# Optimization experiments

Hardware: AMD Instinct MI355X
Metric: run time of the kernel (lower is better)

The kernel has to match this reference:

```python
import jax, jax.numpy as jnp
import numpy as np

NUM_GROUPS, GROUP_SIZE, D_MODEL = 8, 4096, 1024
NUM_EXPERTS = 64
EXPERT_CAPACITY = 1024  # capacity_factor 2: 2 * total_tokens / num_experts


def setup_inputs() -> dict:
    key = jax.random.key(0)
    k1, k2, k3 = jax.random.split(key, 3)
    x = jax.random.normal(k1, (NUM_GROUPS, GROUP_SIZE, D_MODEL), dtype=jnp.float32)
    gate_kernel = jax.random.normal(k2, (D_MODEL, NUM_EXPERTS), dtype=jnp.float32) * 0.1
    gate_bias = jax.random.normal(k3, (NUM_EXPERTS,), dtype=jnp.float32) * 0.01
    temperature = jnp.ones((1,), dtype=jnp.float32)
    return {
        "x": x,
        "gate_kernel": gate_kernel,
        "gate_bias": gate_bias,
        "temperature": temperature,
        "expert_capacity": EXPERT_CAPACITY,
    }


def reference(x, gate_kernel, gate_bias, temperature, expert_capacity):
    # x: [G, S, D]; gate_kernel: [D, E]
    G, S, _ = x.shape
    E = gate_kernel.shape[1]

    router_logits = jnp.einsum("gsd,de->gse", x, gate_kernel) + gate_bias  # [G, S, E]
    safe_temp = jnp.maximum(temperature, 0.1)  # [1]
    router_probs = jax.nn.softmax(router_logits / safe_temp, axis=-1)  # [G, S, E]

    # Per-expert top-k over all flattened tokens.
    flat_probs = router_probs.transpose(2, 0, 1).reshape(E, G * S)  # [E, G*S]
    scores, token_indices = jax.lax.top_k(flat_probs, k=expert_capacity)  # [E, C]

    group_indices = token_indices // S  # [E, C]
    pos_indices = token_indices % S  # [E, C]
    expert_ids = jnp.broadcast_to(jnp.arange(E)[:, None], scores.shape)  # [E, C]

    # use_mask_routing=True path: scatter into capacity-limited dense masks.
    expert_masks = jnp.zeros((E, G, S), dtype=jnp.bool_).at[
        expert_ids, group_indices, pos_indices].set(True)
    weight_masks = jnp.zeros((E, G, S), dtype=x.dtype).at[
        expert_ids, group_indices, pos_indices].set(scores)

    loss = jnp.asarray(0.0, dtype=x.dtype)  # training=False
    return expert_masks, weight_masks, loss
```

## Files before the change

### kernel.cpp

```cpp
#include <hip/hip_runtime.h>
#include <math.h>

#define NG 8
#define SEQ 4096
#define DM 1024
#define NE 64
#define GS (NG * SEQ)
#define KSEL 1024
#define MASK_ELEMS (NE * GS)
#define SEG 16
#define SEGLEN (GS / SEG)
#define CAP 2048
#define CAP2 16384

typedef __attribute__((ext_vector_type(8))) short short8;
typedef __attribute__((ext_vector_type(4))) float f32x4;

__device__ __forceinline__ unsigned short f2bf(float v) {
  unsigned u = __float_as_uint(v);
  return (unsigned short)((u + 0x7FFFu + ((u >> 16) & 1u)) >> 16);
}
__device__ __forceinline__ float bf2f(unsigned short h) {
  return __uint_as_float(((unsigned)h) << 16);
}

__global__ __launch_bounds__(256)
void k_split(const float* __restrict__ w, unsigned short* __restrict__ wph,
             unsigned short* __restrict__ wpm, unsigned* __restrict__ zbase) {
  const int t = blockIdx.x * 256 + threadIdx.x;
  if (t < NE * 256 + NE) zbase[t] = 0u;
  const int k = t >> 6, e = t & 63;
  float v = w[t];
  unsigned short h = f2bf(v); float r = v - bf2f(h);
  const int tile = k >> 5, g = (k >> 3) & 3, j = k & 7;
  const int cb = e >> 4, lrow = e & 15;
  const size_t o = (size_t)(tile * 4 + cb) * 512 + (g * 16 + lrow) * 8 + j;
  wph[o] = h; wpm[o] = f2bf(r);
}

__global__ __launch_bounds__(256, 2)
void k_gemm_softmax(const float* __restrict__ x,
                    const unsigned short* __restrict__ wph,
                    const unsigned short* __restrict__ wpm,
                    const float* __restrict__ bias, const float* __restrict__ temp,
                    float* __restrict__ probsT) {
  __shared__ float Lt[4][64][68];
  float (*Pt)[68] = (float (*)[68])&Lt[0][0][0];

  const int tid = threadIdx.x;
  const int w = tid >> 6, lane = tid & 63;
  const int lrow = lane & 15, g = lane >> 4;
  const int m0 = blockIdx.x * 64;

  int irow[4], jcol[4];
  {
    union { unsigned short u[8]; short8 v; } ar, on;
#pragma unroll
    for (int j = 0; j < 8; ++j) { ar.u[j] = f2bf((float)lrow); on.u[j] = 0x3F80u; }
    f32x4 z = {0.f, 0.f, 0.f, 0.f};
    f32x4 p1 = __builtin_amdgcn_mfma_f32_16x16x32_bf16(ar.v, on.v, z, 0, 0, 0);
    f32x4 p2 = __builtin_amdgcn_mfma_f32_16x16x32_bf16(on.v, ar.v, z, 0, 0, 0);
#pragma unroll
    for (int b = 0; b < 4; ++b) {
      irow[b] = ((int)p1[b]) >> 5;
      jcol[b] = ((int)p2[b]) >> 5;
    }
  }

  f32x4 acc[4][4];
#pragma unroll
  for (int rf = 0; rf < 4; ++rf)
#pragma unroll
    for (int cb = 0; cb < 4; ++cb) acc[rf][cb] = (f32x4){0.f, 0.f, 0.f, 0.f};

  const int boff = lane * 8;
  const int T0 = w * 8;

  f32x4 aP[4][2], aQ[4][2];
  short8 bhP[4], bmP[4], bhQ[4], bmQ[4];

#define LOADA_(T, ar)                                                                \
  {                                                                                  \
    _Pragma("unroll")                                                                \
    for (int rf = 0; rf < 4; ++rf) {                                                 \
      const f32x4* ap = (const f32x4*)(x + (size_t)(m0 + rf * 16 + lrow) * DM +      \
                                       (T) * 32 + g * 8);                            \
      ar[rf][0] = ap[0]; ar[rf][1] = ap[1];                                          \
    }                                                                                \
  }

#define LOADB_(T, bh, bm)                                                            \
  {                                                                                  \
    _Pragma("unroll")                                                                \
    for (int cb = 0; cb < 4; ++cb) {                                                 \
      const size_t bo = (size_t)((T) * 4 + cb) * 512 + boff;                         \
      bh[cb] = *(const short8*)(wph + bo);                                           \
      bm[cb] = *(const short8*)(wpm + bo);                                           \
    }                                                                                \
  }

#define SPLIT_MFMA(ar, bh, bm)                                                       \
  {                                                                                  \
    _Pragma("unroll")                                                                \
    for (int rf = 0; rf < 4; ++rf) {                                                 \
      union { unsigned short u[8]; short8 v; } ah, am;                               \
      _Pragma("unroll")                                                              \
      for (int j = 0; j < 8; ++j) {                                                  \
        float v0 = (j < 4) ? ar[rf][0][j] : ar[rf][1][j - 4];                        \
        unsigned short h_ = f2bf(v0);                                                \
        ah.u[j] = h_; am.u[j] = f2bf(v0 - bf2f(h_));                                 \
      }                                                                              \
      _Pragma("unroll")                                                              \
      for (int cb = 0; cb < 4; ++cb) {                                               \
        acc[rf][cb] = __builtin_amdgcn_mfma_f32_16x16x32_bf16(ah.v, bh[cb],          \
                                                              acc[rf][cb], 0, 0, 0); \
        acc[rf][cb] = __builtin_amdgcn_mfma_f32_16x16x32_bf16(am.v, bh[cb],          \
                                                              acc[rf][cb], 0, 0, 0); \
        acc[rf][cb] = __builtin_amdgcn_mfma_f32_16x16x32_bf16(ah.v, bm[cb],          \
                                                              acc[rf][cb], 0, 0, 0); \
      }                                                                              \
    }                                                                                \
  }

  LOADA_(T0, aP);
  LOADB_(T0, bhP, bmP);
#pragma unroll
  for (int t = 0; t < 8; t += 2) {
    LOADA_(T0 + t + 1, aQ);
    LOADB_(T0 + t + 1, bhQ, bmQ);
    SPLIT_MFMA(aP, bhP, bmP);
    if (t + 2 < 8) {
      LOADA_(T0 + t + 2, aP);
      LOADB_(T0 + t + 2, bhP, bmP);
    }
    SPLIT_MFMA(aQ, bhQ, bmQ);
  }

#undef LOADA_
#undef LOADB_
#undef SPLIT_MFMA

#pragma unroll
  for (int rf = 0; rf < 4; ++rf)
#pragma unroll
    for (int cb = 0; cb < 4; ++cb)
#pragma unroll
      for (int b = 0; b < 4; ++b)
        Lt[w][rf * 16 + irow[b]][cb * 16 + jcol[b]] = acc[rf][cb][b];
  __syncthreads();

  float pr[16];
  const int tk = tid >> 2, q = tid & 3;
  {
    float st = temp[0];
    if (st < 0.1f) st = 0.1f;
    const float inv_t = 1.0f / st;
    float l[16];
    float mx = -1.0e30f;
#pragma unroll
    for (int j = 0; j < 16; ++j) {
      const int e = q * 16 + j;
      l[j] = (Lt[0][tk][e] + Lt[1][tk][e] + Lt[2][tk][e] + Lt[3][tk][e] + bias[e]) *
             inv_t;
      mx = fmaxf(mx, l[j]);
    }
    mx = fmaxf(mx, __shfl_xor(mx, 1));
    mx = fmaxf(mx, __shfl_xor(mx, 2));
    float p[16], s = 0.0f;
#pragma unroll
    for (int j = 0; j < 16; ++j) { p[j] = __expf(l[j] - mx); s += p[j]; }
    s += __shfl_xor(s, 1);
    s += __shfl_xor(s, 2);
    const float invs = 1.0f / s;
#pragma unroll
    for (int j = 0; j < 16; ++j) pr[j] = p[j] * invs;
  }
  __syncthreads();
#pragma unroll
  for (int j = 0; j < 16; ++j) Pt[q * 16 + j][tk] = pr[j];
  __syncthreads();

  {
    const int e = tid >> 2, qq = tid & 3;
    float* dst = probsT + (size_t)e * GS + m0 + qq * 16;
#pragma unroll
    for (int c2 = 0; c2 < 4; ++c2)
      *(float4*)(dst + c2 * 4) = *(const float4*)(&Pt[e][qq * 16 + c2 * 4]);
  }
}

__device__ __forceinline__ void pick_scan(const unsigned* __restrict__ bins,
                                          unsigned r_in, unsigned& bucket,
                                          unsigned& r_out, unsigned* res) {
  __syncthreads();
  const int tid = threadIdx.x;
  if (tid < 64) {
    uint4 b = ((const uint4*)bins)[tid];
    unsigned s3 = b.w, s2 = b.z + s3, s1 = b.y + s2, s0 = b.x + s1;
    unsigned suf = s0;
#pragma unroll
    for (int off = 1; off < 64; off <<= 1) {
      unsigned t = __shfl_down(suf, off);
      if (tid + off < 64) suf += t;
    }
    unsigned above = suf - s0;
    unsigned inc0 = above + s0, inc1 = above + s1, inc2 = above + s2, inc3 = above + s3;
    if (inc3 >= r_in && inc3 - b.w < r_in) { res[0] = 4 * tid + 3; res[1] = r_in - (inc3 - b.w); }
    if (inc2 >= r_in && inc2 - b.z < r_in) { res[0] = 4 * tid + 2; res[1] = r_in - (inc2 - b.z); }
    if (inc1 >= r_in && inc1 - b.y < r_in) { res[0] = 4 * tid + 1; res[1] = r_in - (inc1 - b.y); }
    if (inc0 >= r_in && inc0 - b.x < r_in) { res[0] = 4 * tid + 0; res[1] = r_in - (inc0 - b.x); }
  }
  __syncthreads();
  bucket = res[0];
  r_out = res[1];
}

__global__ __launch_bounds__(256)
void k_hist0(const float* __restrict__ probsT, unsigned* __restrict__ ghist0) {
  __shared__ unsigned h[4][256];
  const int tid = threadIdx.x, wv = tid >> 6;
  const int e = blockIdx.x >> 4;
  const int seg = blockIdx.x & (SEG - 1);
  h[0][tid] = 0; h[1][tid] = 0; h[2][tid] = 0; h[3][tid] = 0;
  __syncthreads();
  const float4* col = (const float4*)(probsT + (size_t)e * GS + seg * SEGLEN);
#pragma unroll
  for (int i = 0; i < SEGLEN / 1024; ++i) {
    float4 v = col[i * 256 + tid];
    atomicAdd(&h[wv][__float_as_uint(v.x) >> 24], 1u);
    atomicAdd(&h[wv][__float_as_uint(v.y) >> 24], 1u);
    atomicAdd(&h[wv][__float_as_uint(v.z) >> 24], 1u);
    atomicAdd(&h[wv][__float_as_uint(v.w) >> 24], 1u);
  }
  __syncthreads();
  unsigned c = h[0][tid] + h[1][tid] + h[2][tid] + h[3][tid];
  if (c) atomicAdd(&ghist0[e * 256 + tid], c);
}

__global__ __launch_bounds__(256)
void k_compact(const float* __restrict__ probsT, const unsigned* __restrict__ ghist0,
               unsigned* __restrict__ cCnt, int* __restrict__ cIdx,
               float* __restrict__ cKey) {
  __shared__ unsigned res[2];
  __shared__ unsigned locN, basePos;
  __shared__ int locIdx[2048];
  __shared__ float locKey[2048];
  const int tid = threadIdx.x;
  const int e = blockIdx.x >> 4;
  const int seg = blockIdx.x & (SEG - 1);

  if (tid == 0) locN = 0u;
  unsigned b0, r0;
  pick_scan(ghist0 + e * 256, KSEL, b0, r0, res);
  const unsigned blo = (b0 == 0u) ? 0u : (b0 - 1u);

  const float* col = probsT + (size_t)e * GS + seg * SEGLEN;
  for (int i = 0; i < SEGLEN / 256; ++i) {
    const int t = i * 256 + tid;
    const float p = col[t];
    if ((__float_as_uint(p) >> 24) >= blo) {
      unsigned pos = atomicAdd(&locN, 1u);
      locIdx[pos] = seg * SEGLEN + t;
      locKey[pos] = p;
    }
  }
  __syncthreads();
  if (tid == 0) basePos = locN ? atomicAdd(&cCnt[e], locN) : 0u;
  __syncthreads();
  const unsigned n = locN, bp = basePos;
  for (unsigned i = tid; i < n; i += 256) {
    const unsigned gp = bp + i;
    if (gp < CAP2) {
      cIdx[(size_t)e * CAP2 + gp] = locIdx[i];
      cKey[(size_t)e * CAP2 + gp] = locKey[i];
    }
  }
}

__global__ __launch_bounds__(256)
void k_select2(const unsigned* __restrict__ ghist0, const unsigned* __restrict__ cCnt,
               const int* __restrict__ cIdx, const float* __restrict__ cKey,
               const float* __restrict__ temp, unsigned* __restrict__ defCnt,
               unsigned* __restrict__ candCnt, int* __restrict__ candIdx,
               float* __restrict__ thrHiA) {
  __shared__ unsigned res[2];
  __shared__ unsigned h[4][256];
  __shared__ unsigned hs[256];
  __shared__ unsigned nd, nc;
  const int tid = threadIdx.x, wv = tid >> 6;
  const int e = blockIdx.x;
  const int cnt = (int)min(cCnt[e], (unsigned)CAP2);

  unsigned b0, r;
  pick_scan(ghist0 + e * 256, KSEL, b0, r, res);
  unsigned pfx = b0 << 24;

  for (int pass = 1; pass < 4; ++pass) {
    const int shift = 24 - 8 * pass;
    const unsigned hm = 0xFFFFFFFFu << (shift + 8);
    for (int i = tid; i < 1024; i += 256) ((unsigned*)h)[i] = 0u;
    __syncthreads();
    for (int i = tid; i < cnt; i += 256) {
      unsigned key = __float_as_uint(cKey[(size_t)e * CAP2 + i]);
      if ((key & hm) == (pfx & hm)) atomicAdd(&h[wv][(key >> shift) & 255], 1u);
    }
    __syncthreads();
    hs[tid] = h[0][tid] + h[1][tid] + h[2][tid] + h[3][tid];
    unsigned b, rn;
    pick_scan(hs, r, b, rn, res);
    pfx |= b << shift;
    r = rn;
  }

  const float thrv = __uint_as_float(pfx);
  float st = temp[0];
  if (st < 0.1f) st = 0.1f;
  const float rel = 2.0e-3f / st;
  const float hi = thrv * (1.0f + rel);
  const float lo = thrv * (1.0f - rel);
  if (tid == 0) thrHiA[e] = hi;

  if (tid == 0) { nd = 0u; nc = 0u; }
  __syncthreads();
  for (int i = tid; i < cnt; i += 256) {
    const float p = cKey[(size_t)e * CAP2 + i];
    const int t = cIdx[(size_t)e * CAP2 + i];
    if (p > hi) {
      atomicAdd(&nd, 1u);
    } else if (p >= lo) {
      unsigned pos = atomicAdd(&nc, 1u);
      if (pos < CAP) candIdx[e * CAP + pos] = t;
    }
  }
  __syncthreads();
  if (tid == 0) {
    defCnt[e] = nd;
    candCnt[e] = min(nc, (unsigned)CAP);
  }
}

__global__ __launch_bounds__(256)
void k_repair(const float* __restrict__ x, const float* __restrict__ w,
              const float* __restrict__ bias, const float* __restrict__ temp,
              const unsigned* __restrict__ candCnt, const int* __restrict__ candIdx,
              double* __restrict__ candKey) {
  __shared__ double red[4][64];
  const int e = blockIdx.x >> 4;
  const int chunk = blockIdx.x & 15;
  const int tid = threadIdx.x;
  const int ee = tid & 63, q = tid >> 6;
  const int cnt = (int)min(candCnt[e], (unsigned)CAP);

  double st = (double)temp[0];
  if (st < 0.1) st = 0.1;
  const double inv_t = 1.0 / st;

  for (int i = chunk; i < cnt; i += 16) {
    const int t = candIdx[e * CAP + i];
    const float* xr = x + (size_t)t * DM;
    double s0 = 0.0, s1 = 0.0, s2 = 0.0, s3 = 0.0;
    const int kb = q * 256;
    for (int k = kb; k < kb + 256; k += 4) {
      s0 += (double)xr[k + 0] * (double)w[(size_t)(k + 0) * NE + ee];
      s1 += (double)xr[k + 1] * (double)w[(size_t)(k + 1) * NE + ee];
      s2 += (double)xr[k + 2] * (double)w[(size_t)(k + 2) * NE + ee];
      s3 += (double)xr[k + 3] * (double)w[(size_t)(k + 3) * NE + ee];
    }
    red[q][ee] = (s0 + s1) + (s2 + s3);
    __syncthreads();
    if (tid < 64) {
      double l = (red[0][tid] + red[1][tid] + red[2][tid] + red[3][tid] +
                  (double)bias[tid]) * inv_t;
      double m = l;
#pragma unroll
      for (int off = 1; off < 64; off <<= 1) m = fmax(m, __shfl_xor(m, off));
      double ex = exp(l - m);
      double ss = ex;
#pragma unroll
      for (int off = 1; off < 64; off <<= 1) ss += __shfl_xor(ss, off);
      if (tid == e) candKey[e * CAP + i] = ex / ss;
    }
    __syncthreads();
  }
}

__global__ __launch_bounds__(256)
void k_scatter(const float* __restrict__ probsT, const float* __restrict__ thrHiA,
               float* __restrict__ out) {
  const int gid = blockIdx.x * 256 + threadIdx.x;
  const int base = gid * 4;
  const int e = base >> 15;
  float4 p = *(const float4*)(probsT + (size_t)base);
  const float hi = thrHiA[e];
  float pv[4] = {p.x, p.y, p.z, p.w};
  float mk[4], wt[4];
#pragma unroll
  for (int c = 0; c < 4; ++c) {
    bool sel = pv[c] > hi;
    mk[c] = sel ? 1.0f : 0.0f;
    wt[c] = sel ? pv[c] : 0.0f;
  }
  *(float4*)(out + (size_t)base) = make_float4(mk[0], mk[1], mk[2], mk[3]);
  *(float4*)(out + (size_t)MASK_ELEMS + base) = make_float4(wt[0], wt[1], wt[2], wt[3]);
  if (gid == 0) out[2 * (size_t)MASK_ELEMS] = 0.0f;
}

__global__ __launch_bounds__(256)
void k_finish(const unsigned* __restrict__ defCnt, const unsigned* __restrict__ candCnt,
              const int* __restrict__ candIdx, const double* __restrict__ candKey,
              const float* __restrict__ probsT, float* __restrict__ out) {
  __shared__ double kd[CAP];
  __shared__ int ti[CAP];
  const int e = blockIdx.x, tid = threadIdx.x;
  const int cnt = (int)min(candCnt[e], (unsigned)CAP);
  const int need = KSEL - (int)defCnt[e];

  for (int i = tid; i < cnt; i += 256) {
    kd[i] = candKey[e * CAP + i];
    ti[i] = candIdx[e * CAP + i];
  }
  __syncthreads();
  for (int i = tid; i < cnt; i += 256) {
    const double ki = kd[i];
    const int tii = ti[i];
    int rank = 0;
    for (int j = 0; j < cnt; ++j)
      rank += (kd[j] > ki) || (kd[j] == ki && ti[j] < tii);
    if (rank < need) {
      out[(size_t)e * GS + tii] = 1.0f;
      out[(size_t)MASK_ELEMS + (size_t)e * GS + tii] = probsT[(size_t)e * GS + tii];
    }
  }
}

extern "C" void kernel_launch(void* const* d_in, const int* in_sizes, int n_in,
                              void* d_out, int out_size, void* d_ws, size_t ws_size,
                              hipStream_t stream) {
  const float* x    = (const float*)d_in[0];
  const float* gw   = (const float*)d_in[1];
  const float* gb   = (const float*)d_in[2];
  const float* temp = (const float*)d_in[3];

  float* probsT    = (float*)d_ws;
  unsigned* ghist0 = (unsigned*)((char*)d_ws + (size_t)MASK_ELEMS * 4);
  unsigned* cCnt   = ghist0 + NE * 256;
  unsigned* defCnt = cCnt + NE;
  unsigned* candCnt = defCnt + NE;
  float* thrHiA    = (float*)(candCnt + NE);
  int* candIdx     = (int*)(thrHiA + NE);
  double* candKey  = (double*)(candIdx + NE * CAP);
  int* cIdx        = (int*)(candKey + NE * CAP);
  float* cKey      = (float*)(cIdx + (size_t)NE * CAP2);
  unsigned short* wph = (unsigned short*)(cKey + (size_t)NE * CAP2);
  unsigned short* wpm = wph + DM * NE;

  k_split<<<DM * NE / 256, 256, 0, stream>>>(gw, wph, wpm, ghist0);
  k_gemm_softmax<<<GS / 64, 256, 0, stream>>>(x, wph, wpm, gb, temp, probsT);
  k_hist0<<<NE * SEG, 256, 0, stream>>>(probsT, ghist0);
  k_compact<<<NE * SEG, 256, 0, stream>>>(probsT, ghist0, cCnt, cIdx, cKey);
  k_select2<<<NE, 256, 0, stream>>>(ghist0, cCnt, cIdx, cKey, temp, defCnt,
                                    candCnt, candIdx, thrHiA);
  k_repair<<<NE * 16, 256, 0, stream>>>(x, gw, gb, temp, candCnt, candIdx, candKey);
  k_scatter<<<MASK_ELEMS / 1024, 256, 0, stream>>>(probsT, thrHiA, (float*)d_out);
  k_finish<<<NE, 256, 0, stream>>>(defCnt, candCnt, candIdx, candKey,
                                   probsT, (float*)d_out);
}
```

Before: 95.20 us.

## Stage x tiles through per-wave LDS double buffer for coalesced global loads

A-operand loads of x now go through a per-wave double-buffered LDS staging area. Each wave reads contiguous 128-byte row segments from global memory, writes them to padded shared memory, and reads back the MFMA fragment layout from LDS. The aim is better global-load coalescing than the old strided per-lane fragment loads. In exchange it adds LDS traffic, a larger shared footprint that may limit occupancy, and an added block barrier before the logits write.

```diff
diff --git a/kernel.cpp b/kernel.cpp
--- a/kernel.cpp
+++ b/kernel.cpp
@@ -44,13 +44,16 @@
                     const unsigned short* __restrict__ wpm,
                     const float* __restrict__ bias, const float* __restrict__ temp,
                     float* __restrict__ probsT) {
-  __shared__ float Lt[4][64][68];
-  float (*Pt)[68] = (float (*)[68])&Lt[0][0][0];
+  __shared__ float S[18432];
+  float (*Lt)[64][68] = (float (*)[64][68])S;
+  float (*Pt)[68] = (float (*)[68])S;
 
   const int tid = threadIdx.x;
   const int w = tid >> 6, lane = tid & 63;
   const int lrow = lane & 15, g = lane >> 4;
   const int m0 = blockIdx.x * 64;
+  const int arow = lane >> 3, acol = (lane & 7) * 4;
+  float* Aw = S + w * 4608;
 
   int irow[4], jcol[4];
   {
@@ -76,17 +79,22 @@
   const int boff = lane * 8;
   const int T0 = w * 8;
 
-  f32x4 aP[4][2], aQ[4][2];
+  f32x4 sreg[8];
   short8 bhP[4], bmP[4], bhQ[4], bmQ[4];
 
-#define LOADA_(T, ar)                                                                \
+#define GLOADA(T)                                                                    \
   {                                                                                  \
     _Pragma("unroll")                                                                \
-    for (int rf = 0; rf < 4; ++rf) {                                                 \
-      const f32x4* ap = (const f32x4*)(x + (size_t)(m0 + rf * 16 + lrow) * DM +      \
-                                       (T) * 32 + g * 8);                            \
-      ar[rf][0] = ap[0]; ar[rf][1] = ap[1];                                          \
-    }                                                                                \
+    for (int i = 0; i < 8; ++i)                                                      \
+      sreg[i] = *(const f32x4*)(x + (size_t)(m0 + i * 8 + arow) * DM +               \
+                                (T) * 32 + acol);                                    \
+  }
+
+#define DSWRITE(buf)                                                                 \
+  {                                                                                  \
+    _Pragma("unroll")                                                                \
+    for (int i = 0; i < 8; ++i)                                                      \
+      *(f32x4*)(Aw + (buf) * 2304 + (i * 8 + arow) * 36 + acol) = sreg[i];           \
   }
 
 #define LOADB_(T, bh, bm)                                                            \
@@ -99,14 +107,16 @@
     }                                                                                \
   }
 
-#define SPLIT_MFMA(ar, bh, bm)                                                       \
+#define FRAG_MFMA(buf, bh, bm)                                                       \
   {                                                                                  \
     _Pragma("unroll")                                                                \
     for (int rf = 0; rf < 4; ++rf) {                                                 \
+      f32x4 lo = *(const f32x4*)(Aw + (buf) * 2304 + (rf * 16 + lrow) * 36 + g * 8); \
+      f32x4 hi = *(const f32x4*)(Aw + (buf) * 2304 + (rf * 16 + lrow) * 36 + g * 8 + 4); \
       union { unsigned short u[8]; short8 v; } ah, am;                               \
       _Pragma("unroll")                                                              \
       for (int j = 0; j < 8; ++j) {                                                  \
-        float v0 = (j < 4) ? ar[rf][0][j] : ar[rf][1][j - 4];                        \
+        float v0 = (j < 4) ? lo[j] : hi[j - 4];                                      \
         unsigned short h_ = f2bf(v0);                                                \
         ah.u[j] = h_; am.u[j] = f2bf(v0 - bf2f(h_));                                 \
       }                                                                              \
@@ -122,23 +132,28 @@
     }                                                                                \
   }
 
-  LOADA_(T0, aP);
+  GLOADA(T0);
+  DSWRITE(0);
   LOADB_(T0, bhP, bmP);
-#pragma unroll
-  for (int t = 0; t < 8; t += 2) {
-    LOADA_(T0 + t + 1, aQ);
-    LOADB_(T0 + t + 1, bhQ, bmQ);
-    SPLIT_MFMA(aP, bhP, bmP);
-    if (t + 2 < 8) {
-      LOADA_(T0 + t + 2, aP);
-      LOADB_(T0 + t + 2, bhP, bmP);
-    }
-    SPLIT_MFMA(aQ, bhQ, bmQ);
-  }
-
-#undef LOADA_
+
+#pragma unroll
+  for (int t = 0; t < 8; ++t) {
+    if (t + 1 < 8) {
+      GLOADA(T0 + t + 1);
+      if (t & 1) { LOADB_(T0 + t + 1, bhP, bmP); }
+      else       { LOADB_(T0 + t + 1, bhQ, bmQ); }
+    }
+    if (t & 1) { FRAG_MFMA(1, bhQ, bmQ); }
+    else       { FRAG_MFMA(0, bhP, bmP); }
+    if (t + 1 < 8) DSWRITE((t + 1) & 1);
+  }
+
+#undef GLOADA
+#undef DSWRITE
 #undef LOADB_
-#undef SPLIT_MFMA
+#undef FRAG_MFMA
+
+  __syncthreads();
 
 #pragma unroll
   for (int rf = 0; rf < 4; ++rf)
```

Result: no change. 94.94 us (-0.3%).

## Restructure router GEMM as single-wave blocks with async global-to-LDS double buffering

Applied to the files above, without the earlier changes.

The GEMM+softmax kernel changes from 4 waves splitting K with a cross-wave LDS reduction to one wave per 64-token block that walks the whole K dimension. Operands are staged through LDS with global_load_lds and double buffering, using explicit vmcnt waits so loads overlap the split-bf16 MFMAs. Softmax is now computed straight from the accumulators with lane shuffles, which removes the reduction buffer and two barriers. The trade-off is a longer serial K loop per wave and fewer waves per block, so latency hiding depends on occupancy across blocks, and the hand-written waitcnt counts must match the issued loads exactly.

```diff
diff --git a/kernel.cpp b/kernel.cpp
--- a/kernel.cpp
+++ b/kernel.cpp
@@ -24,6 +24,11 @@
   return __uint_as_float(((unsigned)h) << 16);
 }
 
+#define GLDS(gsrc, ldst)                                                             \
+  __builtin_amdgcn_global_load_lds(                                                  \
+      (const __attribute__((address_space(1))) void*)(gsrc),                         \
+      (__attribute__((address_space(3))) void*)(ldst), 16, 0, 0)
+
 __global__ __launch_bounds__(256)
 void k_split(const float* __restrict__ w, unsigned short* __restrict__ wph,
              unsigned short* __restrict__ wpm, unsigned* __restrict__ zbase) {
@@ -38,17 +43,17 @@
   wph[o] = h; wpm[o] = f2bf(r);
 }
 
-__global__ __launch_bounds__(256, 2)
+__global__ __launch_bounds__(64)
 void k_gemm_softmax(const float* __restrict__ x,
                     const unsigned short* __restrict__ wph,
                     const unsigned short* __restrict__ wpm,
                     const float* __restrict__ bias, const float* __restrict__ temp,
                     float* __restrict__ probsT) {
-  __shared__ float Lt[4][64][68];
-  float (*Pt)[68] = (float (*)[68])&Lt[0][0][0];
-
-  const int tid = threadIdx.x;
-  const int w = tid >> 6, lane = tid & 63;
+  __shared__ float S[8192];
+  float (*Pt)[68] = (float (*)[68])S;
+  float* Sf = S;
+
+  const int lane = threadIdx.x;
   const int lrow = lane & 15, g = lane >> 4;
   const int m0 = blockIdx.x * 64;
 
@@ -73,119 +78,112 @@
 #pragma unroll
     for (int cb = 0; cb < 4; ++cb) acc[rf][cb] = (f32x4){0.f, 0.f, 0.f, 0.f};
 
-  const int boff = lane * 8;
-  const int T0 = w * 8;
-
-  f32x4 aP[4][2], aQ[4][2];
-  short8 bhP[4], bmP[4], bhQ[4], bmQ[4];
-
-#define LOADA_(T, ar)                                                                \
+#define ISSUE(T, buf)                                                                \
   {                                                                                  \
     _Pragma("unroll")                                                                \
-    for (int rf = 0; rf < 4; ++rf) {                                                 \
-      const f32x4* ap = (const f32x4*)(x + (size_t)(m0 + rf * 16 + lrow) * DM +      \
-                                       (T) * 32 + g * 8);                            \
-      ar[rf][0] = ap[0]; ar[rf][1] = ap[1];                                          \
+    for (int q = 0; q < 8; ++q) {                                                    \
+      const int c = q * 64 + lane;                                                   \
+      const int gg = c >> 7, row = (c >> 1) & 63, half = c & 1;                      \
+      const float* gsrc = x + (size_t)(m0 + row) * DM + (T) * 32 + gg * 8 + half * 4;\
+      GLDS(gsrc, Sf + (buf) * 4096 + q * 256);                                       \
     }                                                                                \
-  }
-
-#define LOADB_(T, bh, bm)                                                            \
+    _Pragma("unroll")                                                                \
+    for (int q = 0; q < 8; ++q) {                                                    \
+      const unsigned short* bp = (q < 4) ? wph : wpm;                                \
+      const unsigned short* gsrc = bp + (size_t)((T) * 4 + (q & 3)) * 512 + lane * 8;\
+      GLDS(gsrc, Sf + (buf) * 4096 + 2048 + q * 256);                                \
+    }                                                                                \
+  }
+
+#define COMPUTE(buf)                                                                 \
   {                                                                                  \
-    _Pragma("unroll")                                                                \
-    for (int cb = 0; cb < 4; ++cb) {                                                 \
-      const size_t bo = (size_t)((T) * 4 + cb) * 512 + boff;                         \
-      bh[cb] = *(const short8*)(wph + bo);                                           \
-      bm[cb] = *(const short8*)(wpm + bo);                                           \
-    }                                                                                \
-  }
-
-#define SPLIT_MFMA(ar, bh, bm)                                                       \
-  {                                                                                  \
+    const unsigned short* bb = (const unsigned short*)(Sf + (buf) * 4096 + 2048);    \
     _Pragma("unroll")                                                                \
     for (int rf = 0; rf < 4; ++rf) {                                                 \
+      const float* ab = Sf + (buf) * 4096 + g * 512 + (rf * 16 + lrow) * 8;          \
+      f32x4 lo = *(const f32x4*)ab;                                                  \
+      f32x4 hi = *(const f32x4*)(ab + 4);                                            \
       union { unsigned short u[8]; short8 v; } ah, am;                               \
       _Pragma("unroll")                                                              \
       for (int j = 0; j < 8; ++j) {                                                  \
-        float v0 = (j < 4) ? ar[rf][0][j] : ar[rf][1][j - 4];                        \
+        float v0 = (j < 4) ? lo[j] : hi[j - 4];                                      \
         unsigned short h_ = f2bf(v0);                                                \
         ah.u[j] = h_; am.u[j] = f2bf(v0 - bf2f(h_));                                 \
       }                                                                              \
       _Pragma("unroll")                                                              \
       for (int cb = 0; cb < 4; ++cb) {                                               \
-        acc[rf][cb] = __builtin_amdgcn_mfma_f32_16x16x32_bf16(ah.v, bh[cb],          \
+        short8 bh_ = *(const short8*)(bb + cb * 512 + lane * 8);                     \
+        short8 bm_ = *(const short8*)(bb + 2048 + cb * 512 + lane * 8);              \
+        acc[rf][cb] = __builtin_amdgcn_mfma_f32_16x16x32_bf16(ah.v, bh_,             \
                                                               acc[rf][cb], 0, 0, 0); \
-        acc[rf][cb] = __builtin_amdgcn_mfma_f32_16x16x32_bf16(am.v, bh[cb],          \
+        acc[rf][cb] = __builtin_amdgcn_mfma_f32_16x16x32_bf16(am.v, bh_,             \
                                                               acc[rf][cb], 0, 0, 0); \
-        acc[rf][cb] = __builtin_amdgcn_mfma_f32_16x16x32_bf16(ah.v, bm[cb],          \
+        acc[rf][cb] = __builtin_amdgcn_mfma_f32_16x16x32_bf16(ah.v, bm_,             \
                                                               acc[rf][cb], 0, 0, 0); \
       }                                                                              \
     }                                                                                \
   }
 
-  LOADA_(T0, aP);
-  LOADB_(T0, bhP, bmP);
-#pragma unroll
-  for (int t = 0; t < 8; t += 2) {
-    LOADA_(T0 + t + 1, aQ);
-    LOADB_(T0 + t + 1, bhQ, bmQ);
-    SPLIT_MFMA(aP, bhP, bmP);
-    if (t + 2 < 8) {
-      LOADA_(T0 + t + 2, aP);
-      LOADB_(T0 + t + 2, bhP, bmP);
-    }
-    SPLIT_MFMA(aQ, bhQ, bmQ);
-  }
-
-#undef LOADA_
-#undef LOADB_
-#undef SPLIT_MFMA
-
-#pragma unroll
-  for (int rf = 0; rf < 4; ++rf)
-#pragma unroll
-    for (int cb = 0; cb < 4; ++cb)
-#pragma unroll
-      for (int b = 0; b < 4; ++b)
-        Lt[w][rf * 16 + irow[b]][cb * 16 + jcol[b]] = acc[rf][cb][b];
-  __syncthreads();
-
-  float pr[16];
-  const int tk = tid >> 2, q = tid & 3;
+#define WAIT16 { asm volatile("s_waitcnt vmcnt(16)" ::: "memory");                   \
+                 __builtin_amdgcn_sched_barrier(0); }
+#define WAIT0  { asm volatile("s_waitcnt vmcnt(0)" ::: "memory");                    \
+                 __builtin_amdgcn_sched_barrier(0); }
+
+  ISSUE(0, 0);
+  ISSUE(1, 1);
+  for (int t = 0; t < 30; ++t) {
+    WAIT16;
+    COMPUTE(t & 1);
+    __builtin_amdgcn_sched_barrier(0);
+    ISSUE(t + 2, t & 1);
+  }
+  WAIT16; COMPUTE(0);
+  WAIT0;  COMPUTE(1);
+
+#undef ISSUE
+#undef COMPUTE
+#undef WAIT16
+#undef WAIT0
+
   {
     float st = temp[0];
     if (st < 0.1f) st = 0.1f;
     const float inv_t = 1.0f / st;
-    float l[16];
-    float mx = -1.0e30f;
-#pragma unroll
-    for (int j = 0; j < 16; ++j) {
-      const int e = q * 16 + j;
-      l[j] = (Lt[0][tk][e] + Lt[1][tk][e] + Lt[2][tk][e] + Lt[3][tk][e] + bias[e]) *
-             inv_t;
-      mx = fmaxf(mx, l[j]);
-    }
-    mx = fmaxf(mx, __shfl_xor(mx, 1));
-    mx = fmaxf(mx, __shfl_xor(mx, 2));
-    float p[16], s = 0.0f;
-#pragma unroll
-    for (int j = 0; j < 16; ++j) { p[j] = __expf(l[j] - mx); s += p[j]; }
-    s += __shfl_xor(s, 1);
-    s += __shfl_xor(s, 2);
-    const float invs = 1.0f / s;
-#pragma unroll
-    for (int j = 0; j < 16; ++j) pr[j] = p[j] * invs;
-  }
-  __syncthreads();
-#pragma unroll
-  for (int j = 0; j < 16; ++j) Pt[q * 16 + j][tk] = pr[j];
-  __syncthreads();
-
-  {
-    const int e = tid >> 2, qq = tid & 3;
-    float* dst = probsT + (size_t)e * GS + m0 + qq * 16;
-#pragma unroll
-    for (int c2 = 0; c2 < 4; ++c2)
-      *(float4*)(dst + c2 * 4) = *(const float4*)(&Pt[e][qq * 16 + c2 * 4]);
+#pragma unroll
+    for (int rf = 0; rf < 4; ++rf) {
+#pragma unroll
+      for (int b = 0; b < 4; ++b) {
+        float l[4];
+        float mx = -1.0e30f;
+#pragma unroll
+        for (int cb = 0; cb < 4; ++cb) {
+          l[cb] = (acc[rf][cb][b] + bias[cb * 16 + jcol[b]]) * inv_t;
+          mx = fmaxf(mx, l[cb]);
+        }
+        mx = fmaxf(mx, __shfl_xor(mx, 1));
+        mx = fmaxf(mx, __shfl_xor(mx, 2));
+        mx = fmaxf(mx, __shfl_xor(mx, 4));
+        mx = fmaxf(mx, __shfl_xor(mx, 8));
+        float p[4], s = 0.0f;
+#pragma unroll
+        for (int cb = 0; cb < 4; ++cb) { p[cb] = __expf(l[cb] - mx); s += p[cb]; }
+        s += __shfl_xor(s, 1);
+        s += __shfl_xor(s, 2);
+        s += __shfl_xor(s, 4);
+        s += __shfl_xor(s, 8);
+        const float invs = 1.0f / s;
+#pragma unroll
+        for (int cb = 0; cb < 4; ++cb)
+          Pt[cb * 16 + jcol[b]][rf * 16 + irow[b]] = p[cb] * invs;
+      }
+    }
+  }
+
+#pragma unroll
+  for (int it = 0; it < 16; ++it) {
+    const int e = it * 4 + (lane >> 4);
+    const int tok = (lane & 15) * 4;
+    *(float4*)(probsT + (size_t)e * GS + m0 + tok) = *(const float4*)(&Pt[e][tok]);
   }
 }
 
@@ -455,7 +453,7 @@
   unsigned short* wpm = wph + DM * NE;
 
   k_split<<<DM * NE / 256, 256, 0, stream>>>(gw, wph, wpm, ghist0);
-  k_gemm_softmax<<<GS / 64, 256, 0, stream>>>(x, wph, wpm, gb, temp, probsT);
+  k_gemm_softmax<<<GS / 64, 64, 0, stream>>>(x, wph, wpm, gb, temp, probsT);
   k_hist0<<<NE * SEG, 256, 0, stream>>>(probsT, ghist0);
   k_compact<<<NE * SEG, 256, 0, stream>>>(probsT, ghist0, cCnt, cIdx, cKey);
   k_select2<<<NE, 256, 0, stream>>>(ghist0, cCnt, cIdx, cKey, temp, defCnt,
```

After: 112.4 us. 1.18x slower.
